# Kernel tuning notes

Hardware: AMD Instinct MI355X
Metric: run time of the kernel (lower is better)

## Reference

```python
import jax, jax.numpy as jnp
import numpy as np
import math

B, S, H = 2, 2048, 2048
NH, HD = 16, 128           # num_heads, head_dim; num_kv_heads == num_heads (MHA)
THETA = 10000.0


def setup_inputs() -> dict:
    key = jax.random.key(0)
    ks = jax.random.split(key, 5)
    scale = 0.02
    hidden_states = jax.random.normal(ks[0], (B, S, H), jnp.float32)
    q_w = jax.random.normal(ks[1], (H, H), jnp.float32) * scale
    k_w = jax.random.normal(ks[2], (H, H), jnp.float32) * scale
    v_w = jax.random.normal(ks[3], (H, H), jnp.float32) * scale
    o_w = jax.random.normal(ks[4], (H, H), jnp.float32) * scale
    # additive causal mask, finite large-negative (as HF builds it)
    causal = jnp.tril(jnp.ones((S, S), bool))
    attention_mask = jnp.where(causal, 0.0, -1e9).astype(jnp.float32)[None, None]  # [1,1,S,S]
    position_ids = jnp.broadcast_to(jnp.arange(S, dtype=jnp.int64), (B, S))
    return {
        "hidden_states": hidden_states,
        "q_w": q_w, "k_w": k_w, "v_w": v_w, "o_w": o_w,
        "attention_mask": attention_mask,
        "position_ids": position_ids,
    }


def _rotate_half(x):
    x1, x2 = x[..., : x.shape[-1] // 2], x[..., x.shape[-1] // 2 :]
    return jnp.concatenate((-x2, x1), axis=-1)


def _rope_cos_sin(position_ids):
    inv_freq = 1.0 / (THETA ** (jnp.arange(0, HD, 2, dtype=jnp.float32) / HD))  # [HD/2]
    freqs = position_ids.astype(jnp.float32)[:, :, None] * inv_freq[None, None, :]  # [B,S,HD/2]
    emb = jnp.concatenate((freqs, freqs), axis=-1)  # [B,S,HD]
    # unsqueeze head dim (unsqueeze_dim=1 after transpose to [B,H,S,D])
    return jnp.cos(emb)[:, None], jnp.sin(emb)[:, None]  # [B,1,S,HD]


def reference(hidden_states, q_w, k_w, v_w, o_w, attention_mask, position_ids):
    # projections (torch Linear: y = x @ W^T), split heads -> [B,NH,S,HD]
    def proj(w):
        return jnp.einsum('bsh,oh->bso', hidden_states, w).reshape(B, S, NH, HD).transpose(0, 2, 1, 3)
    q, k, v = proj(q_w), proj(k_w), proj(v_w)

    cos, sin = _rope_cos_sin(position_ids)
    q = q * cos + _rotate_half(q) * sin
    k = k * cos + _rotate_half(k) * sin

    scores = jnp.einsum('bhqd,bhkd->bhqk', q, k) / math.sqrt(HD)  # [B,NH,S,S]
    scores = scores + attention_mask
    attn = jax.nn.softmax(scores, axis=-1)  # dropout p=0.0 -> identity
    out = jnp.einsum('bhqk,bhkd->bhqd', attn, v)  # [B,NH,S,HD]
    out = out.transpose(0, 2, 1, 3).reshape(B, S, H)
    return jnp.einsum('bsh,oh->bso', out, o_w)
```

## Files before the change

kernel.cpp:

```cpp
#include <hip/hip_runtime.h>
#include <hip/hip_bf16.h>

using bf16 = __hip_bfloat16;
typedef short  short8  __attribute__((ext_vector_type(8)));
typedef float  float4_ __attribute__((ext_vector_type(4)));
typedef int    int4_   __attribute__((ext_vector_type(4)));

typedef __attribute__((address_space(1))) const void* gas_ptr;
typedef __attribute__((address_space(3))) void*       las_ptr;

#define MFMA_BF16(a, b, c) __builtin_amdgcn_mfma_f32_16x16x32_bf16((a), (b), (c), 0, 0, 0)

__device__ __forceinline__ float bf2f(bf16 v) { return __bfloat162float(v); }
__device__ __forceinline__ bf16  f2bf(float v) { return __float2bfloat16(v); }

#define BAR() do { asm volatile("" ::: "memory"); __builtin_amdgcn_s_barrier(); asm volatile("" ::: "memory"); } while (0)
#define WAITLGKM0() asm volatile("s_waitcnt lgkmcnt(0)" ::: "memory")

template<int CTRL>
__device__ __forceinline__ float dppmv(float x) {
    return __int_as_float(__builtin_amdgcn_update_dpp(
        0, __float_as_int(x), CTRL, 0xF, 0xF, true));
}
__device__ __forceinline__ float row16_max(float x) {
    x = fmaxf(x, dppmv<0xB1>(x));
    x = fmaxf(x, dppmv<0x4E>(x));
    x = fmaxf(x, dppmv<0x124>(x));
    x = fmaxf(x, dppmv<0x128>(x));
    return x;
}
__device__ __forceinline__ float row16_sum(float x) {
    x += dppmv<0xB1>(x);
    x += dppmv<0x4E>(x);
    x += dppmv<0x124>(x);
    x += dppmv<0x128>(x);
    return x;
}

__global__ __launch_bounds__(256)
void cvt_all(const float* __restrict__ X,  const float* __restrict__ Wq,
             const float* __restrict__ Wk, const float* __restrict__ Wv,
             const float* __restrict__ Wo,
             bf16* __restrict__ Xb,  bf16* __restrict__ Wqb,
             bf16* __restrict__ Wkb, bf16* __restrict__ Wvb,
             bf16* __restrict__ Wob)
{
    const size_t i = ((size_t)blockIdx.x * 256 + threadIdx.x) * 8;
    const float* src; bf16* dst; size_t off;
    if (i < 8388608)       { src = X;  dst = Xb;  off = i; }
    else if (i < 12582912) { src = Wq; dst = Wqb; off = i - 8388608; }
    else if (i < 16777216) { src = Wk; dst = Wkb; off = i - 12582912; }
    else if (i < 20971520) { src = Wv; dst = Wvb; off = i - 16777216; }
    else                   { src = Wo; dst = Wob; off = i - 20971520; }
    const float4_ a = *(const float4_*)(src + off);
    const float4_ b = *(const float4_*)(src + off + 4);
    union { short8 s; bf16 h[8]; } u;
#pragma unroll
    for (int j = 0; j < 4; ++j) { u.h[j] = f2bf(a[j]); u.h[j + 4] = f2bf(b[j]); }
    *(short8*)(dst + off) = u.s;
}

__global__ __launch_bounds__(512, 2)
void gemm_bn128(const bf16* __restrict__ Ap, const bf16* __restrict__ Wp,
                bf16* __restrict__ Oq, float* __restrict__ OF, int mode)
{
    constexpr int NT = 32;
    __shared__ bf16 As0[2 * 256 * 64];
    __shared__ bf16 Bs0[2 * 128 * 64];

    const int nwg  = gridDim.x * gridDim.y;
    const int bid0 = blockIdx.y * gridDim.x + blockIdx.x;
    const int cpx  = nwg >> 3;
    const int swzb = (bid0 & 7) * cpx + (bid0 >> 3);
    const int bn = (swzb % gridDim.x) * 128;
    const int bm = (swzb / gridDim.x) * 256;

    const int tid  = threadIdx.x;
    const int w    = tid >> 6;
    const int ln   = tid & 63;
    const int r15  = ln & 15;
    const int quad = ln >> 4;
    const int wr   = w >> 1;
    const int wc   = w & 1;

    const int srow = ln >> 3;
    const int scol = ((ln & 7) ^ srow) * 8;
    const int w8   = w * 8;
    const int cx   = (r15 & 7) * 8;

#define STAGE_A(pb, ts) do {                                                \
    _Pragma("unroll")                                                       \
    for (int c = 0; c < 4; ++c) {                                           \
        const int rl = c * 64 + w8;                                         \
        __builtin_amdgcn_global_load_lds(                                   \
            (gas_ptr)(Ap + (size_t)(bm + rl + srow) * 2048 + (ts) * 64 + scol), \
            (las_ptr)(As0 + (pb) * 16384 + rl * 64), 16, 0, 0);             \
    } } while (0)

#define STAGE_B0(pb, ts) do {                                               \
    const int rl = w8;                                                      \
    __builtin_amdgcn_global_load_lds(                                       \
        (gas_ptr)(Wp + (size_t)(bn + rl + srow) * 2048 + (ts) * 64 + scol), \
        (las_ptr)(Bs0 + (pb) * 8192 + rl * 64), 16, 0, 0);                  \
    } while (0)

#define STAGE_B1(pb, ts) do {                                               \
    const int rl = 64 + w8;                                                 \
    __builtin_amdgcn_global_load_lds(                                       \
        (gas_ptr)(Wp + (size_t)(bn + rl + srow) * 2048 + (ts) * 64 + scol), \
        (las_ptr)(Bs0 + (pb) * 8192 + rl * 64), 16, 0, 0);                  \
    } while (0)

#define LDA() do {                                                          \
    _Pragma("unroll")                                                       \
    for (int mi = 0; mi < 4; ++mi) {                                        \
        const int row = wr * 64 + mi * 16 + r15;                            \
        a[mi][0] = *(const short8*)(As0 + p * 16384 + row * 64 + ((quad * 8) ^ cx));      \
        a[mi][1] = *(const short8*)(As0 + p * 16384 + row * 64 + ((32 + quad * 8) ^ cx)); \
    } } while (0)

#define LDB(qn) do {                                                        \
    _Pragma("unroll")                                                       \
    for (int j = 0; j < 2; ++j) {                                           \
        const int row = wc * 64 + ((qn) * 2 + j) * 16 + r15;                \
        b[j][0] = *(const short8*)(Bs0 + p * 8192 + row * 64 + ((quad * 8) ^ cx));      \
        b[j][1] = *(const short8*)(Bs0 + p * 8192 + row * 64 + ((32 + quad * 8) ^ cx)); \
    } } while (0)

#define MM(qn) do {                                                         \
    __builtin_amdgcn_s_setprio(1);                                          \
    _Pragma("unroll")                                                       \
    for (int mi = 0; mi < 4; ++mi)                                          \
        _Pragma("unroll")                                                   \
        for (int j = 0; j < 2; ++j)                                         \
            _Pragma("unroll")                                               \
            for (int kk = 0; kk < 2; ++kk)                                  \
                acc[mi][(qn) * 2 + j] =                                     \
                    MFMA_BF16(a[mi][kk], b[j][kk], acc[mi][(qn) * 2 + j]);  \
    __builtin_amdgcn_s_setprio(0); } while (0)

    float4_ acc[4][4];
    const float4_ fzero = {0.f, 0.f, 0.f, 0.f};
#pragma unroll
    for (int i = 0; i < 4; ++i)
#pragma unroll
        for (int j = 0; j < 4; ++j) acc[i][j] = fzero;

    short8 a[4][2], b[2][2];

    STAGE_A(0, 0); STAGE_B0(0, 0); STAGE_B1(0, 0);
    STAGE_A(1, 1); STAGE_B0(1, 1);
    asm volatile("s_waitcnt vmcnt(5)" ::: "memory");
    BAR();

    for (int t = 0; t < NT; ++t) {
        const int p = t & 1, pq = p ^ 1;
        LDA(); LDB(0);
        if (t + 1 < NT) STAGE_B1(pq, t + 1);
        asm volatile("s_waitcnt lgkmcnt(8)" ::: "memory");
        BAR(); WAITLGKM0();
        MM(0);
        BAR();
        LDB(1);
        if (t + 2 < NT) { STAGE_A(p, t + 2); STAGE_B0(p, t + 2); }
        BAR(); WAITLGKM0();
        MM(1);
        if (t >= NT - 2) { asm volatile("s_waitcnt vmcnt(0)" ::: "memory"); }
        else             { asm volatile("s_waitcnt vmcnt(5)" ::: "memory"); }
        BAR();
    }

#pragma unroll
    for (int mi = 0; mi < 4; ++mi) {
#pragma unroll
        for (int ni = 0; ni < 4; ++ni) {
#pragma unroll
            for (int r = 0; r < 4; ++r) {
                const int row = bm + wr * 64 + mi * 16 + quad * 4 + r;
                const int col = bn + wc * 64 + ni * 16 + r15;
                const float v = acc[mi][ni][r];
                if (mode == 0) {
                    const int z = col >> 11, c2 = col & 2047;
                    const int h = c2 >> 7, d = c2 & 127;
                    const int bb = row >> 11, s = row & 2047;
                    Oq[(size_t)z * 8388608 + (((size_t)bb * 16 + h) * 2048 + s) * 128 + d] = f2bf(v);
                } else {
                    OF[(size_t)row * 2048 + col] = v;
                }
            }
        }
    }
#undef STAGE_A
#undef STAGE_B0
#undef STAGE_B1
#undef LDA
#undef LDB
#undef MM
}

__global__ __launch_bounds__(256)
void rope_scale(bf16* __restrict__ Q, bf16* __restrict__ Kb)
{
    const int idx = blockIdx.x * 256 + threadIdx.x;
    const int d  = idx & 63;
    const int s  = (idx >> 6) & 2047;
    const int bh = idx >> 17;
    const size_t base = ((size_t)bh * 2048 + s) * 128;

    const float inv_freq = expf(-(float)d * (9.210340371976184f / 64.f));
    const float ang = (float)s * inv_freq;
    const float c = cosf(ang), sn = sinf(ang);
    const float sc = 0.08838834764831845f;

    const float q1 = bf2f(Q[base + d]), q2 = bf2f(Q[base + d + 64]);
    Q[base + d]      = f2bf((q1 * c - q2 * sn) * sc);
    Q[base + d + 64] = f2bf((q2 * c + q1 * sn) * sc);

    const float k1 = bf2f(Kb[base + d]), k2 = bf2f(Kb[base + d + 64]);
    Kb[base + d]      = f2bf(k1 * c - k2 * sn);
    Kb[base + d + 64] = f2bf(k2 * c + k1 * sn);
}

__global__ __launch_bounds__(512)
void flash_attn(const bf16* __restrict__ Qg, const bf16* __restrict__ Kg,
                const bf16* __restrict__ Vg, bf16* __restrict__ Og)
{
    constexpr int S = 2048;
    const int pr = blockIdx.x;
    const int bh = blockIdx.y;
    const int b = bh >> 4, h = bh & 15;
    const size_t base = (size_t)bh * S * 128;
    const bf16* Qp = Qg + base;
    const bf16* Kp = Kg + base;
    const bf16* Vp = Vg + base;

    const int tid  = threadIdx.x;
    const int wave = tid >> 6;
    const int ln   = tid & 63;
    const int r15  = ln & 15;
    const int quad = ln >> 4;
    const int sid  = wave & 3;
    const int hi   = wave >> 2;

    __shared__ bf16 Ks[64][136];
    __shared__ bf16 Vt[128][72];
    __shared__ bf16 Ps[8][32][72];

    const int strip = hi ? (15 - pr) : pr;
    const int qrow0 = strip * 128 + sid * 32;
    const int dt    = qrow0 >> 6;
    const int ktmax = 2 * (15 - pr) + 1;

    short8 qf[2][4];
#pragma unroll
    for (int rf = 0; rf < 2; ++rf)
#pragma unroll
        for (int ks = 0; ks < 4; ++ks)
            qf[rf][ks] = *(const short8*)&Qp[(size_t)(qrow0 + rf * 16 + r15) * 128
                                             + ks * 32 + quad * 8];

    float4_ acc_o[2][8];
    const float4_ fzero = {0.f, 0.f, 0.f, 0.f};
#pragma unroll
    for (int rf = 0; rf < 2; ++rf)
#pragma unroll
        for (int of = 0; of < 8; ++of) acc_o[rf][of] = fzero;
    float m_run[2][4], l_run[2][4];
#pragma unroll
    for (int rf = 0; rf < 2; ++rf)
#pragma unroll
        for (int r = 0; r < 4; ++r) { m_run[rf][r] = -__builtin_inff(); l_run[rf][r] = 0.f; }

    const int kr = tid >> 4;
    const int kc = (tid & 15) * 8;
    const int vd = wave * 16;

    {
#pragma unroll
        for (int p = 0; p < 2; ++p)
            *(int4_*)&Ks[kr + p * 32][kc] =
                *(const int4_*)&Kp[(size_t)(kr + p * 32) * 128 + kc];
        union { int4_ v; bf16 h[8]; } u;
#pragma unroll
        for (int p = 0; p < 2; ++p) {
            u.v = *(const int4_*)&Vp[(size_t)ln * 128 + vd + p * 8];
#pragma unroll
            for (int j = 0; j < 8; ++j)
                Vt[vd + p * 8 + j][ln] = u.h[j];
        }
    }
    __syncthreads();

    for (int kt = 0; kt <= ktmax; ++kt) {
        const bool more = (kt < ktmax);

        int4_ kpre0, kpre1, vpre0, vpre1;
        if (more) {
            const int krow = (kt + 1) * 64;
            kpre0 = *(const int4_*)&Kp[(size_t)(krow + kr) * 128 + kc];
            kpre1 = *(const int4_*)&Kp[(size_t)(krow + kr + 32) * 128 + kc];
            vpre0 = *(const int4_*)&Vp[(size_t)(krow + ln) * 128 + vd];
            vpre1 = *(const int4_*)&Vp[(size_t)(krow + ln) * 128 + vd + 8];
        }

        if (kt <= dt) {
            float4_ sacc[2][4];
            __builtin_amdgcn_s_setprio(1);
#pragma unroll
            for (int nf = 0; nf < 4; ++nf) {
                sacc[0][nf] = fzero;
                sacc[1][nf] = fzero;
#pragma unroll
                for (int ks = 0; ks < 4; ++ks) {
                    short8 kf = *(const short8*)&Ks[nf * 16 + r15][ks * 32 + quad * 8];
                    sacc[0][nf] = MFMA_BF16(qf[0][ks], kf, sacc[0][nf]);
                    sacc[1][nf] = MFMA_BF16(qf[1][ks], kf, sacc[1][nf]);
                }
            }
            __builtin_amdgcn_s_setprio(0);

            if (kt == dt) {
#pragma unroll
                for (int rf = 0; rf < 2; ++rf) {
                    const int ro = (qrow0 & 63) + rf * 16 + quad * 4;
#pragma unroll
                    for (int nf = 0; nf < 4; ++nf) {
                        const int col = nf * 16 + r15;
#pragma unroll
                        for (int r = 0; r < 4; ++r)
                            if (col > ro + r) sacc[rf][nf][r] = -__builtin_inff();
                    }
                }
            }

#pragma unroll
            for (int rf = 0; rf < 2; ++rf) {
                float rm4[4];
                float g = 0.f;
#pragma unroll
                for (int r = 0; r < 4; ++r) {
                    float rm = fmaxf(fmaxf(sacc[rf][0][r], sacc[rf][1][r]),
                                     fmaxf(sacc[rf][2][r], sacc[rf][3][r]));
                    rm4[r] = row16_max(rm);
                    g = fmaxf(g, rm4[r] - m_run[rf][r]);
                }
                const bool resc = !__all(g <= 8.f);
                float mnew[4], alpha[4];
                if (resc) {
#pragma unroll
                    for (int r = 0; r < 4; ++r) {
                        mnew[r]  = fmaxf(m_run[rf][r], rm4[r]);
                        alpha[r] = __expf(m_run[rf][r] - mnew[r]);
                        m_run[rf][r] = mnew[r];
                    }
                } else {
#pragma unroll
                    for (int r = 0; r < 4; ++r) { mnew[r] = m_run[rf][r]; alpha[r] = 1.f; }
                }
                float rs[4] = {0.f, 0.f, 0.f, 0.f};
#pragma unroll
                for (int nf = 0; nf < 4; ++nf) {
#pragma unroll
                    for (int r = 0; r < 4; ++r) {
                        const float pp = __expf(sacc[rf][nf][r] - mnew[r]);
                        rs[r] += pp;
                        Ps[wave][rf * 16 + quad * 4 + r][nf * 16 + r15] = f2bf(pp);
                    }
                }
#pragma unroll
                for (int r = 0; r < 4; ++r) {
                    const float t = row16_sum(rs[r]);
                    l_run[rf][r] = resc ? (l_run[rf][r] * alpha[r] + t)
                                        : (l_run[rf][r] + t);
                }
                if (resc) {
#pragma unroll
                    for (int of = 0; of < 8; ++of)
#pragma unroll
                        for (int r = 0; r < 4; ++r)
                            acc_o[rf][of][r] *= alpha[r];
                }
            }

            __builtin_amdgcn_s_setprio(1);
#pragma unroll
            for (int k2 = 0; k2 < 2; ++k2) {
                short8 pf0 = *(const short8*)&Ps[wave][r15][k2 * 32 + quad * 8];
                short8 pf1 = *(const short8*)&Ps[wave][16 + r15][k2 * 32 + quad * 8];
#pragma unroll
                for (int of = 0; of < 8; ++of) {
                    short8 vf = *(const short8*)&Vt[of * 16 + r15][k2 * 32 + quad * 8];
                    acc_o[0][of] = MFMA_BF16(pf0, vf, acc_o[0][of]);
                    acc_o[1][of] = MFMA_BF16(pf1, vf, acc_o[1][of]);
                }
            }
            __builtin_amdgcn_s_setprio(0);
        }

        __syncthreads();
        if (more) {
            *(int4_*)&Ks[kr][kc]      = kpre0;
            *(int4_*)&Ks[kr + 32][kc] = kpre1;
            union { int4_ v; bf16 h[8]; } u;
            u.v = vpre0;
#pragma unroll
            for (int j = 0; j < 8; ++j) Vt[vd + j][ln] = u.h[j];
            u.v = vpre1;
#pragma unroll
            for (int j = 0; j < 8; ++j) Vt[vd + 8 + j][ln] = u.h[j];
        }
        __syncthreads();
    }

#pragma unroll
    for (int rf = 0; rf < 2; ++rf) {
#pragma unroll
        for (int r = 0; r < 4; ++r) {
            const float inv = 1.f / l_run[rf][r];
            const int  s  = qrow0 + rf * 16 + quad * 4 + r;
            const size_t ob = (((size_t)b * S + s) * 16 + h) * 128;
#pragma unroll
            for (int of = 0; of < 8; ++of)
                Og[ob + of * 16 + r15] = f2bf(acc_o[rf][of][r] * inv);
        }
    }
}

extern "C" void kernel_launch(void* const* d_in, const int* in_sizes, int n_in,
                              void* d_out, int out_size, void* d_ws, size_t ws_size,
                              hipStream_t stream)
{
    const float* X  = (const float*)d_in[0];
    const float* Wq = (const float*)d_in[1];
    const float* Wk = (const float*)d_in[2];
    const float* Wv = (const float*)d_in[3];
    const float* Wo = (const float*)d_in[4];
    float* out = (float*)d_out;

    bf16* Xb  = (bf16*)d_ws;
    bf16* Wqb = Xb  + 8388608;
    bf16* Wkb = Wqb + 4194304;
    bf16* Wvb = Wkb + 4194304;
    bf16* Wob = Wvb + 4194304;
    bf16* q   = Wob + 4194304;
    bf16* k   = q   + 8388608;
    bf16* v   = k   + 8388608;
    bf16* ao  = v   + 8388608;

    dim3 blk(256);
    cvt_all<<<dim3(12288), blk, 0, stream>>>(X, Wq, Wk, Wv, Wo,
                                             Xb, Wqb, Wkb, Wvb, Wob);
    gemm_bn128<<<dim3(48, 16), dim3(512), 0, stream>>>(Xb, Wqb, q, nullptr, 0);
    rope_scale<<<dim3((2 * 16 * 2048 * 64) / 256), blk, 0, stream>>>(q, k);
    flash_attn<<<dim3(8, 32), dim3(512), 0, stream>>>(q, k, v, ao);
    gemm_bn128<<<dim3(16, 16), dim3(512), 0, stream>>>(ao, Wob, nullptr, out, 1);
}
```

Measured before the change: 421.7 us.

## Restructure flash attention into 256-thread blocks pairing 64-row strips; tabulate RoPE

Flash attention now launches 16x32 blocks of 4 waves. Each wave handles a 16-row slice of a low query strip and a 16-row slice of its mirrored high strip, and the high strip alone keeps running after the low strip hits its diagonal, which keeps causal work balanced at a finer 64-row granularity. K/V staging is spread across fewer threads, each doing more loads. A separate kernel precomputes a RoPE cos/sin table so rope_scale does not call expf/sinf/cosf per element, at the cost of an extra launch and table reads. The smaller blocks and extra grid may change occupancy and double the K/V reload traffic per head.

```diff
diff --git a/kernel.cpp b/kernel.cpp
--- a/kernel.cpp
+++ b/kernel.cpp
@@ -199,7 +199,19 @@
 }
 
 __global__ __launch_bounds__(256)
-void rope_scale(bf16* __restrict__ Q, bf16* __restrict__ Kb)
+void rope_tab(float2* __restrict__ tab)
+{
+    const int i = blockIdx.x * 256 + threadIdx.x;
+    const int d = i & 63;
+    const int s = i >> 6;
+    const float inv_freq = expf(-(float)d * (9.210340371976184f / 64.f));
+    const float ang = (float)s * inv_freq;
+    tab[i] = make_float2(cosf(ang), sinf(ang));
+}
+
+__global__ __launch_bounds__(256)
+void rope_scale(bf16* __restrict__ Q, bf16* __restrict__ Kb,
+                const float2* __restrict__ tab)
 {
     const int idx = blockIdx.x * 256 + threadIdx.x;
     const int d  = idx & 63;
@@ -207,9 +219,8 @@
     const int bh = idx >> 17;
     const size_t base = ((size_t)bh * 2048 + s) * 128;
 
-    const float inv_freq = expf(-(float)d * (9.210340371976184f / 64.f));
-    const float ang = (float)s * inv_freq;
-    const float c = cosf(ang), sn = sinf(ang);
+    const float2 cs = tab[s * 64 + d];
+    const float c = cs.x, sn = cs.y;
     const float sc = 0.08838834764831845f;
 
     const float q1 = bf2f(Q[base + d]), q2 = bf2f(Q[base + d + 64]);
@@ -221,12 +232,12 @@
     Kb[base + d + 64] = f2bf(k2 * c + k1 * sn);
 }
 
-__global__ __launch_bounds__(512)
+__global__ __launch_bounds__(256)
 void flash_attn(const bf16* __restrict__ Qg, const bf16* __restrict__ Kg,
                 const bf16* __restrict__ Vg, bf16* __restrict__ Og)
 {
     constexpr int S = 2048;
-    const int pr = blockIdx.x;
+    const int p  = blockIdx.x;
     const int bh = blockIdx.y;
     const int b = bh >> 4, h = bh & 15;
     const size_t base = (size_t)bh * S * 128;
@@ -239,25 +250,23 @@
     const int ln   = tid & 63;
     const int r15  = ln & 15;
     const int quad = ln >> 4;
-    const int sid  = wave & 3;
-    const int hi   = wave >> 2;
 
     __shared__ bf16 Ks[64][136];
     __shared__ bf16 Vt[128][72];
-    __shared__ bf16 Ps[8][32][72];
-
-    const int strip = hi ? (15 - pr) : pr;
-    const int qrow0 = strip * 128 + sid * 32;
-    const int dt    = qrow0 >> 6;
-    const int ktmax = 2 * (15 - pr) + 1;
+    __shared__ bf16 Ps[4][32][72];
+
+    const int qlo   = p * 64 + wave * 16;
+    const int qhi   = (31 - p) * 64 + wave * 16;
+    const int dtlo  = p;
+    const int ktmax = 31 - p;
+    const int ro    = wave * 16 + quad * 4;
 
     short8 qf[2][4];
 #pragma unroll
-    for (int rf = 0; rf < 2; ++rf)
-#pragma unroll
-        for (int ks = 0; ks < 4; ++ks)
-            qf[rf][ks] = *(const short8*)&Qp[(size_t)(qrow0 + rf * 16 + r15) * 128
-                                             + ks * 32 + quad * 8];
+    for (int ks = 0; ks < 4; ++ks) {
+        qf[0][ks] = *(const short8*)&Qp[(size_t)(qlo + r15) * 128 + ks * 32 + quad * 8];
+        qf[1][ks] = *(const short8*)&Qp[(size_t)(qhi + r15) * 128 + ks * 32 + quad * 8];
+    }
 
     float4_ acc_o[2][8];
     const float4_ fzero = {0.f, 0.f, 0.f, 0.f};
@@ -273,43 +282,96 @@
 
     const int kr = tid >> 4;
     const int kc = (tid & 15) * 8;
-    const int vd = wave * 16;
+    const int vd = wave * 32;
 
     {
 #pragma unroll
-        for (int p = 0; p < 2; ++p)
-            *(int4_*)&Ks[kr + p * 32][kc] =
-                *(const int4_*)&Kp[(size_t)(kr + p * 32) * 128 + kc];
+        for (int pp = 0; pp < 4; ++pp)
+            *(int4_*)&Ks[kr + pp * 16][kc] =
+                *(const int4_*)&Kp[(size_t)(kr + pp * 16) * 128 + kc];
         union { int4_ v; bf16 h[8]; } u;
 #pragma unroll
-        for (int p = 0; p < 2; ++p) {
-            u.v = *(const int4_*)&Vp[(size_t)ln * 128 + vd + p * 8];
+        for (int pp = 0; pp < 4; ++pp) {
+            u.v = *(const int4_*)&Vp[(size_t)ln * 128 + vd + pp * 8];
 #pragma unroll
             for (int j = 0; j < 8; ++j)
-                Vt[vd + p * 8 + j][ln] = u.h[j];
+                Vt[vd + pp * 8 + j][ln] = u.h[j];
         }
     }
     __syncthreads();
+
+#define SOFTMAX(rfi) do {                                                   \
+        float rm4[4]; float g = 0.f;                                        \
+        _Pragma("unroll")                                                   \
+        for (int r = 0; r < 4; ++r) {                                       \
+            float rm = fmaxf(fmaxf(sacc[rfi][0][r], sacc[rfi][1][r]),       \
+                             fmaxf(sacc[rfi][2][r], sacc[rfi][3][r]));      \
+            rm4[r] = row16_max(rm);                                         \
+            g = fmaxf(g, rm4[r] - m_run[rfi][r]);                           \
+        }                                                                   \
+        const bool resc = !__all(g <= 8.f);                                 \
+        float mnew[4];                                                      \
+        if (resc) {                                                         \
+            float alpha[4];                                                 \
+            _Pragma("unroll")                                               \
+            for (int r = 0; r < 4; ++r) {                                   \
+                mnew[r]  = fmaxf(m_run[rfi][r], rm4[r]);                    \
+                alpha[r] = __expf(m_run[rfi][r] - mnew[r]);                 \
+                m_run[rfi][r] = mnew[r];                                    \
+            }                                                               \
+            _Pragma("unroll")                                               \
+            for (int r = 0; r < 4; ++r) l_run[rfi][r] *= alpha[r];          \
+            _Pragma("unroll")                                               \
+            for (int of = 0; of < 8; ++of)                                  \
+                _Pragma("unroll")                                           \
+                for (int r = 0; r < 4; ++r)                                 \
+                    acc_o[rfi][of][r] *= alpha[r];                          \
+        } else {                                                            \
+            _Pragma("unroll")                                               \
+            for (int r = 0; r < 4; ++r) mnew[r] = m_run[rfi][r];            \
+        }                                                                   \
+        float rs[4] = {0.f, 0.f, 0.f, 0.f};                                 \
+        _Pragma("unroll")                                                   \
+        for (int nf = 0; nf < 4; ++nf)                                      \
+            _Pragma("unroll")                                               \
+            for (int r = 0; r < 4; ++r) {                                   \
+                const float pp2 = __expf(sacc[rfi][nf][r] - mnew[r]);       \
+                rs[r] += pp2;                                               \
+                Ps[wave][(rfi) * 16 + quad * 4 + r][nf * 16 + r15] = f2bf(pp2); \
+            }                                                               \
+        _Pragma("unroll")                                                   \
+        for (int r = 0; r < 4; ++r) l_run[rfi][r] += row16_sum(rs[r]);      \
+    } while (0)
+
+#define DIAGMASK(rfi) do {                                                  \
+        _Pragma("unroll")                                                   \
+        for (int nf = 0; nf < 4; ++nf) {                                    \
+            const int col = nf * 16 + r15;                                  \
+            _Pragma("unroll")                                               \
+            for (int r = 0; r < 4; ++r)                                     \
+                if (col > ro + r) sacc[rfi][nf][r] = -__builtin_inff();     \
+        }                                                                   \
+    } while (0)
 
     for (int kt = 0; kt <= ktmax; ++kt) {
         const bool more = (kt < ktmax);
 
-        int4_ kpre0, kpre1, vpre0, vpre1;
+        int4_ kpre[4], vpre[4];
         if (more) {
             const int krow = (kt + 1) * 64;
-            kpre0 = *(const int4_*)&Kp[(size_t)(krow + kr) * 128 + kc];
-            kpre1 = *(const int4_*)&Kp[(size_t)(krow + kr + 32) * 128 + kc];
-            vpre0 = *(const int4_*)&Vp[(size_t)(krow + ln) * 128 + vd];
-            vpre1 = *(const int4_*)&Vp[(size_t)(krow + ln) * 128 + vd + 8];
-        }
-
-        if (kt <= dt) {
-            float4_ sacc[2][4];
+#pragma unroll
+            for (int pp = 0; pp < 4; ++pp) {
+                kpre[pp] = *(const int4_*)&Kp[(size_t)(krow + kr + pp * 16) * 128 + kc];
+                vpre[pp] = *(const int4_*)&Vp[(size_t)(krow + ln) * 128 + vd + pp * 8];
+            }
+        }
+
+        float4_ sacc[2][4];
+        if (kt <= dtlo) {
             __builtin_amdgcn_s_setprio(1);
 #pragma unroll
             for (int nf = 0; nf < 4; ++nf) {
-                sacc[0][nf] = fzero;
-                sacc[1][nf] = fzero;
+                sacc[0][nf] = fzero; sacc[1][nf] = fzero;
 #pragma unroll
                 for (int ks = 0; ks < 4; ++ks) {
                     short8 kf = *(const short8*)&Ks[nf * 16 + r15][ks * 32 + quad * 8];
@@ -318,70 +380,9 @@
                 }
             }
             __builtin_amdgcn_s_setprio(0);
-
-            if (kt == dt) {
-#pragma unroll
-                for (int rf = 0; rf < 2; ++rf) {
-                    const int ro = (qrow0 & 63) + rf * 16 + quad * 4;
-#pragma unroll
-                    for (int nf = 0; nf < 4; ++nf) {
-                        const int col = nf * 16 + r15;
-#pragma unroll
-                        for (int r = 0; r < 4; ++r)
-                            if (col > ro + r) sacc[rf][nf][r] = -__builtin_inff();
-                    }
-                }
-            }
-
-#pragma unroll
-            for (int rf = 0; rf < 2; ++rf) {
-                float rm4[4];
-                float g = 0.f;
-#pragma unroll
-                for (int r = 0; r < 4; ++r) {
-                    float rm = fmaxf(fmaxf(sacc[rf][0][r], sacc[rf][1][r]),
-                                     fmaxf(sacc[rf][2][r], sacc[rf][3][r]));
-                    rm4[r] = row16_max(rm);
-                    g = fmaxf(g, rm4[r] - m_run[rf][r]);
-                }
-                const bool resc = !__all(g <= 8.f);
-                float mnew[4], alpha[4];
-                if (resc) {
-#pragma unroll
-                    for (int r = 0; r < 4; ++r) {
-                        mnew[r]  = fmaxf(m_run[rf][r], rm4[r]);
-                        alpha[r] = __expf(m_run[rf][r] - mnew[r]);
-                        m_run[rf][r] = mnew[r];
-                    }
-                } else {
-#pragma unroll
-                    for (int r = 0; r < 4; ++r) { mnew[r] = m_run[rf][r]; alpha[r] = 1.f; }
-                }
-                float rs[4] = {0.f, 0.f, 0.f, 0.f};
-#pragma unroll
-                for (int nf = 0; nf < 4; ++nf) {
-#pragma unroll
-                    for (int r = 0; r < 4; ++r) {
-                        const float pp = __expf(sacc[rf][nf][r] - mnew[r]);
-                        rs[r] += pp;
-                        Ps[wave][rf * 16 + quad * 4 + r][nf * 16 + r15] = f2bf(pp);
-                    }
-                }
-#pragma unroll
-                for (int r = 0; r < 4; ++r) {
-                    const float t = row16_sum(rs[r]);
-                    l_run[rf][r] = resc ? (l_run[rf][r] * alpha[r] + t)
-                                        : (l_run[rf][r] + t);
-                }
-                if (resc) {
-#pragma unroll
-                    for (int of = 0; of < 8; ++of)
-#pragma unroll
-                        for (int r = 0; r < 4; ++r)
-                            acc_o[rf][of][r] *= alpha[r];
-                }
-            }
-
+            if (kt == dtlo) DIAGMASK(0);
+            SOFTMAX(0);
+            SOFTMAX(1);
             __builtin_amdgcn_s_setprio(1);
 #pragma unroll
             for (int k2 = 0; k2 < 2; ++k2) {
@@ -395,29 +396,58 @@
                 }
             }
             __builtin_amdgcn_s_setprio(0);
+        } else {
+            __builtin_amdgcn_s_setprio(1);
+#pragma unroll
+            for (int nf = 0; nf < 4; ++nf) {
+                sacc[1][nf] = fzero;
+#pragma unroll
+                for (int ks = 0; ks < 4; ++ks) {
+                    short8 kf = *(const short8*)&Ks[nf * 16 + r15][ks * 32 + quad * 8];
+                    sacc[1][nf] = MFMA_BF16(qf[1][ks], kf, sacc[1][nf]);
+                }
+            }
+            __builtin_amdgcn_s_setprio(0);
+            if (kt == ktmax) DIAGMASK(1);
+            SOFTMAX(1);
+            __builtin_amdgcn_s_setprio(1);
+#pragma unroll
+            for (int k2 = 0; k2 < 2; ++k2) {
+                short8 pf1 = *(const short8*)&Ps[wave][16 + r15][k2 * 32 + quad * 8];
+#pragma unroll
+                for (int of = 0; of < 8; ++of) {
+                    short8 vf = *(const short8*)&Vt[of * 16 + r15][k2 * 32 + quad * 8];
+                    acc_o[1][of] = MFMA_BF16(pf1, vf, acc_o[1][of]);
+                }
+            }
+            __builtin_amdgcn_s_setprio(0);
         }
 
         __syncthreads();
         if (more) {
-            *(int4_*)&Ks[kr][kc]      = kpre0;
-            *(int4_*)&Ks[kr + 32][kc] = kpre1;
+#pragma unroll
+            for (int pp = 0; pp < 4; ++pp)
+                *(int4_*)&Ks[kr + pp * 16][kc] = kpre[pp];
             union { int4_ v; bf16 h[8]; } u;
-            u.v = vpre0;
-#pragma unroll
-            for (int j = 0; j < 8; ++j) Vt[vd + j][ln] = u.h[j];
-            u.v = vpre1;
-#pragma unroll
-            for (int j = 0; j < 8; ++j) Vt[vd + 8 + j][ln] = u.h[j];
+#pragma unroll
+            for (int pp = 0; pp < 4; ++pp) {
+                u.v = vpre[pp];
+#pragma unroll
+                for (int j = 0; j < 8; ++j) Vt[vd + pp * 8 + j][ln] = u.h[j];
+            }
         }
         __syncthreads();
     }
+#undef SOFTMAX
+#undef DIAGMASK
 
 #pragma unroll
     for (int rf = 0; rf < 2; ++rf) {
+        const int q0 = rf ? qhi : qlo;
 #pragma unroll
         for (int r = 0; r < 4; ++r) {
             const float inv = 1.f / l_run[rf][r];
-            const int  s  = qrow0 + rf * 16 + quad * 4 + r;
+            const int  s  = q0 + quad * 4 + r;
             const size_t ob = (((size_t)b * S + s) * 16 + h) * 128;
 #pragma unroll
             for (int of = 0; of < 8; ++of)
@@ -446,12 +476,14 @@
     bf16* k   = q   + 8388608;
     bf16* v   = k   + 8388608;
     bf16* ao  = v   + 8388608;
+    float2* tab = (float2*)(ao + 8388608);
 
     dim3 blk(256);
+    rope_tab<<<dim3(512), blk, 0, stream>>>(tab);
     cvt_all<<<dim3(12288), blk, 0, stream>>>(X, Wq, Wk, Wv, Wo,
                                              Xb, Wqb, Wkb, Wvb, Wob);
     gemm_bn128<<<dim3(48, 16), dim3(512), 0, stream>>>(Xb, Wqb, q, nullptr, 0);
-    rope_scale<<<dim3((2 * 16 * 2048 * 64) / 256), blk, 0, stream>>>(q, k);
-    flash_attn<<<dim3(8, 32), dim3(512), 0, stream>>>(q, k, v, ao);
+    rope_scale<<<dim3((2 * 16 * 2048 * 64) / 256), blk, 0, stream>>>(q, k, tab);
+    flash_attn<<<dim3(16, 32), blk, 0, stream>>>(q, k, v, ao);
     gemm_bn128<<<dim3(16, 16), dim3(512), 0, stream>>>(ao, Wob, nullptr, out, 1);
 }
```

Result: slower. 487.6 us (+15.6%).

## Split GEMM k-step into four quadrant MFMA phases and precompute RoPE table

Applied to the files above, without the earlier changes.

The GEMM main loop now loads A and B fragments in halves and issues four 2x2 MFMA quadrants, interleaving the next-stage global-to-LDS loads (B0, B1, A) between them. The aim is smaller LDS read bursts and more even overlap of memory and compute, at the cost of extra barriers per k-step. Separately, a small kernel precomputes the cos/sin table once per call, so rope_scale reads it instead of evaluating expf/cosf/sinf for every element. This adds one extra launch and a table read.

```diff
diff --git a/kernel.cpp b/kernel.cpp
--- a/kernel.cpp
+++ b/kernel.cpp
@@ -111,32 +111,32 @@
         (las_ptr)(Bs0 + (pb) * 8192 + rl * 64), 16, 0, 0);                  \
     } while (0)
 
-#define LDA() do {                                                          \
-    _Pragma("unroll")                                                       \
-    for (int mi = 0; mi < 4; ++mi) {                                        \
-        const int row = wr * 64 + mi * 16 + r15;                            \
-        a[mi][0] = *(const short8*)(As0 + p * 16384 + row * 64 + ((quad * 8) ^ cx));      \
-        a[mi][1] = *(const short8*)(As0 + p * 16384 + row * 64 + ((32 + quad * 8) ^ cx)); \
-    } } while (0)
-
-#define LDB(qn) do {                                                        \
+#define LDA_H(dst, hm) do {                                                 \
     _Pragma("unroll")                                                       \
     for (int j = 0; j < 2; ++j) {                                           \
-        const int row = wc * 64 + ((qn) * 2 + j) * 16 + r15;                \
-        b[j][0] = *(const short8*)(Bs0 + p * 8192 + row * 64 + ((quad * 8) ^ cx));      \
-        b[j][1] = *(const short8*)(Bs0 + p * 8192 + row * 64 + ((32 + quad * 8) ^ cx)); \
+        const int row = wr * 64 + ((hm) * 2 + j) * 16 + r15;                \
+        dst[j][0] = *(const short8*)(As0 + p * 16384 + row * 64 + ((quad * 8) ^ cx));      \
+        dst[j][1] = *(const short8*)(As0 + p * 16384 + row * 64 + ((32 + quad * 8) ^ cx)); \
     } } while (0)
 
-#define MM(qn) do {                                                         \
+#define LDB_H(dst, hn) do {                                                 \
+    _Pragma("unroll")                                                       \
+    for (int j = 0; j < 2; ++j) {                                           \
+        const int row = wc * 64 + ((hn) * 2 + j) * 16 + r15;                \
+        dst[j][0] = *(const short8*)(Bs0 + p * 8192 + row * 64 + ((quad * 8) ^ cx));      \
+        dst[j][1] = *(const short8*)(Bs0 + p * 8192 + row * 64 + ((32 + quad * 8) ^ cx)); \
+    } } while (0)
+
+#define MMQ(am, bnv, mo, no) do {                                           \
     __builtin_amdgcn_s_setprio(1);                                          \
     _Pragma("unroll")                                                       \
-    for (int mi = 0; mi < 4; ++mi)                                          \
+    for (int i = 0; i < 2; ++i)                                             \
         _Pragma("unroll")                                                   \
         for (int j = 0; j < 2; ++j)                                         \
             _Pragma("unroll")                                               \
             for (int kk = 0; kk < 2; ++kk)                                  \
-                acc[mi][(qn) * 2 + j] =                                     \
-                    MFMA_BF16(a[mi][kk], b[j][kk], acc[mi][(qn) * 2 + j]);  \
+                acc[(mo) * 2 + i][(no) * 2 + j] =                           \
+                    MFMA_BF16(am[i][kk], bnv[j][kk], acc[(mo) * 2 + i][(no) * 2 + j]); \
     __builtin_amdgcn_s_setprio(0); } while (0)
 
     float4_ acc[4][4];
@@ -146,27 +146,34 @@
 #pragma unroll
         for (int j = 0; j < 4; ++j) acc[i][j] = fzero;
 
-    short8 a[4][2], b[2][2];
+    short8 a0[2][2], a1[2][2], b0[2][2], b1[2][2];
 
     STAGE_A(0, 0); STAGE_B0(0, 0); STAGE_B1(0, 0);
-    STAGE_A(1, 1); STAGE_B0(1, 1);
-    asm volatile("s_waitcnt vmcnt(5)" ::: "memory");
+    STAGE_A(1, 1); STAGE_B0(1, 1); STAGE_B1(1, 1);
+    asm volatile("s_waitcnt vmcnt(6)" ::: "memory");
     BAR();
 
     for (int t = 0; t < NT; ++t) {
-        const int p = t & 1, pq = p ^ 1;
-        LDA(); LDB(0);
-        if (t + 1 < NT) STAGE_B1(pq, t + 1);
-        asm volatile("s_waitcnt lgkmcnt(8)" ::: "memory");
+        const int p = t & 1;
+        LDA_H(a0, 0); LDB_H(b0, 0);
         BAR(); WAITLGKM0();
-        MM(0);
+        MMQ(a0, b0, 0, 0);
         BAR();
-        LDB(1);
-        if (t + 2 < NT) { STAGE_A(p, t + 2); STAGE_B0(p, t + 2); }
+        LDB_H(b1, 1);
+        if (t + 2 < NT) STAGE_B0(p, t + 2);
         BAR(); WAITLGKM0();
-        MM(1);
+        MMQ(a0, b1, 0, 1);
+        BAR();
+        LDA_H(a1, 1);
+        if (t + 2 < NT) STAGE_B1(p, t + 2);
+        BAR(); WAITLGKM0();
+        MMQ(a1, b1, 1, 1);
+        BAR();
+        if (t + 2 < NT) STAGE_A(p, t + 2);
+        BAR();
+        MMQ(a1, b0, 1, 0);
         if (t >= NT - 2) { asm volatile("s_waitcnt vmcnt(0)" ::: "memory"); }
-        else             { asm volatile("s_waitcnt vmcnt(5)" ::: "memory"); }
+        else             { asm volatile("s_waitcnt vmcnt(6)" ::: "memory"); }
         BAR();
     }
 
@@ -193,13 +200,25 @@
 #undef STAGE_A
 #undef STAGE_B0
 #undef STAGE_B1
-#undef LDA
-#undef LDB
-#undef MM
+#undef LDA_H
+#undef LDB_H
+#undef MMQ
 }
 
 __global__ __launch_bounds__(256)
-void rope_scale(bf16* __restrict__ Q, bf16* __restrict__ Kb)
+void rope_tab(float2* __restrict__ tab)
+{
+    const int i = blockIdx.x * 256 + threadIdx.x;
+    const int d = i & 63;
+    const int s = i >> 6;
+    const float inv_freq = expf(-(float)d * (9.210340371976184f / 64.f));
+    const float ang = (float)s * inv_freq;
+    tab[i] = make_float2(cosf(ang), sinf(ang));
+}
+
+__global__ __launch_bounds__(256)
+void rope_scale(bf16* __restrict__ Q, bf16* __restrict__ Kb,
+                const float2* __restrict__ tab)
 {
     const int idx = blockIdx.x * 256 + threadIdx.x;
     const int d  = idx & 63;
@@ -207,9 +226,8 @@
     const int bh = idx >> 17;
     const size_t base = ((size_t)bh * 2048 + s) * 128;
 
-    const float inv_freq = expf(-(float)d * (9.210340371976184f / 64.f));
-    const float ang = (float)s * inv_freq;
-    const float c = cosf(ang), sn = sinf(ang);
+    const float2 cs = tab[s * 64 + d];
+    const float c = cs.x, sn = cs.y;
     const float sc = 0.08838834764831845f;
 
     const float q1 = bf2f(Q[base + d]), q2 = bf2f(Q[base + d + 64]);
@@ -446,12 +464,14 @@
     bf16* k   = q   + 8388608;
     bf16* v   = k   + 8388608;
     bf16* ao  = v   + 8388608;
+    float2* tab = (float2*)(ao + 8388608);
 
     dim3 blk(256);
+    rope_tab<<<dim3(512), blk, 0, stream>>>(tab);
     cvt_all<<<dim3(12288), blk, 0, stream>>>(X, Wq, Wk, Wv, Wo,
                                              Xb, Wqb, Wkb, Wvb, Wob);
     gemm_bn128<<<dim3(48, 16), dim3(512), 0, stream>>>(Xb, Wqb, q, nullptr, 0);
-    rope_scale<<<dim3((2 * 16 * 2048 * 64) / 256), blk, 0, stream>>>(q, k);
+    rope_scale<<<dim3((2 * 16 * 2048 * 64) / 256), blk, 0, stream>>>(q, k, tab);
     flash_attn<<<dim3(8, 32), dim3(512), 0, stream>>>(q, k, v, ao);
     gemm_bn128<<<dim3(16, 16), dim3(512), 0, stream>>>(ao, Wob, nullptr, out, 1);
 }
```

Result: slower. 470.2 us (+11.5%).

## Fuse RoPE and query scaling into the QKV GEMM epilogue via a cos/sin table

Applied to the files above, without the earlier changes.

Drops the separate rope_scale kernel, which re-read and re-wrote the whole Q and K tensors. The QKV GEMM's B-tile columns are remapped so each wave holds both the d and d+64 halves of a head, and its epilogue applies the rotation (plus the query scale for Q) before storing bf16. A 2048x64 cos/sin table is built by extra blocks appended to the conversion kernel, which avoids transcendental math in the GEMM epilogue. This saves one kernel launch and a full memory round trip, at the cost of a heavier epilogue with table loads and branches.

```diff
diff --git a/kernel.cpp b/kernel.cpp
--- a/kernel.cpp
+++ b/kernel.cpp
@@ -43,8 +43,17 @@
              const float* __restrict__ Wo,
              bf16* __restrict__ Xb,  bf16* __restrict__ Wqb,
              bf16* __restrict__ Wkb, bf16* __restrict__ Wvb,
-             bf16* __restrict__ Wob)
+             bf16* __restrict__ Wob, float2* __restrict__ tab)
 {
+    if (blockIdx.x >= 12288) {
+        const int i = (blockIdx.x - 12288) * 256 + threadIdx.x;
+        const int d = i & 63;
+        const int s = i >> 6;
+        const float inv_freq = expf(-(float)d * (9.210340371976184f / 64.f));
+        const float ang = (float)s * inv_freq;
+        tab[i] = make_float2(cosf(ang), sinf(ang));
+        return;
+    }
     const size_t i = ((size_t)blockIdx.x * 256 + threadIdx.x) * 8;
     const float* src; bf16* dst; size_t off;
     if (i < 8388608)       { src = X;  dst = Xb;  off = i; }
@@ -62,7 +71,8 @@
 
 __global__ __launch_bounds__(512, 2)
 void gemm_bn128(const bf16* __restrict__ Ap, const bf16* __restrict__ Wp,
-                bf16* __restrict__ Oq, float* __restrict__ OF, int mode)
+                bf16* __restrict__ Oq, float* __restrict__ OF,
+                const float2* __restrict__ tab, int mode)
 {
     constexpr int NT = 32;
     __shared__ bf16 As0[2 * 256 * 64];
@@ -122,7 +132,7 @@
 #define LDB(qn) do {                                                        \
     _Pragma("unroll")                                                       \
     for (int j = 0; j < 2; ++j) {                                           \
-        const int row = wc * 64 + ((qn) * 2 + j) * 16 + r15;                \
+        const int row = wc * 32 + (qn) * 64 + j * 16 + r15;                 \
         b[j][0] = *(const short8*)(Bs0 + p * 8192 + row * 64 + ((quad * 8) ^ cx));      \
         b[j][1] = *(const short8*)(Bs0 + p * 8192 + row * 64 + ((32 + quad * 8) ^ cx)); \
     } } while (0)
@@ -170,22 +180,45 @@
         BAR();
     }
 
-#pragma unroll
-    for (int mi = 0; mi < 4; ++mi) {
-#pragma unroll
-        for (int ni = 0; ni < 4; ++ni) {
-#pragma unroll
-            for (int r = 0; r < 4; ++r) {
-                const int row = bm + wr * 64 + mi * 16 + quad * 4 + r;
-                const int col = bn + wc * 64 + ni * 16 + r15;
-                const float v = acc[mi][ni][r];
-                if (mode == 0) {
-                    const int z = col >> 11, c2 = col & 2047;
-                    const int h = c2 >> 7, d = c2 & 127;
+    if (mode == 0) {
+        const int z = bn >> 11;
+        const int h = (bn >> 7) & 15;
+        bf16* Ob = Oq + (size_t)z * 8388608;
+        const float sc = 0.08838834764831845f;
+#pragma unroll
+        for (int mi = 0; mi < 4; ++mi) {
+#pragma unroll
+            for (int ni = 0; ni < 2; ++ni) {
+                const int d = wc * 32 + ni * 16 + r15;
+#pragma unroll
+                for (int r = 0; r < 4; ++r) {
+                    const int row = bm + wr * 64 + mi * 16 + quad * 4 + r;
                     const int bb = row >> 11, s = row & 2047;
-                    Oq[(size_t)z * 8388608 + (((size_t)bb * 16 + h) * 2048 + s) * 128 + d] = f2bf(v);
-                } else {
-                    OF[(size_t)row * 2048 + col] = v;
+                    float vlo = acc[mi][ni][r];
+                    float vhi = acc[mi][ni + 2][r];
+                    if (z < 2) {
+                        const float2 cs = tab[s * 64 + d];
+                        const float lo = vlo * cs.x - vhi * cs.y;
+                        const float hi = vhi * cs.x + vlo * cs.y;
+                        vlo = lo; vhi = hi;
+                        if (z == 0) { vlo *= sc; vhi *= sc; }
+                    }
+                    const size_t ob = (((size_t)bb * 16 + h) * 2048 + s) * 128 + d;
+                    Ob[ob]      = f2bf(vlo);
+                    Ob[ob + 64] = f2bf(vhi);
+                }
+            }
+        }
+    } else {
+#pragma unroll
+        for (int mi = 0; mi < 4; ++mi) {
+#pragma unroll
+            for (int ni = 0; ni < 4; ++ni) {
+                const int col = bn + wc * 32 + (ni >> 1) * 64 + (ni & 1) * 16 + r15;
+#pragma unroll
+                for (int r = 0; r < 4; ++r) {
+                    const int row = bm + wr * 64 + mi * 16 + quad * 4 + r;
+                    OF[(size_t)row * 2048 + col] = acc[mi][ni][r];
                 }
             }
         }
@@ -196,29 +229,6 @@
 #undef LDA
 #undef LDB
 #undef MM
-}
-
-__global__ __launch_bounds__(256)
-void rope_scale(bf16* __restrict__ Q, bf16* __restrict__ Kb)
-{
-    const int idx = blockIdx.x * 256 + threadIdx.x;
-    const int d  = idx & 63;
-    const int s  = (idx >> 6) & 2047;
-    const int bh = idx >> 17;
-    const size_t base = ((size_t)bh * 2048 + s) * 128;
-
-    const float inv_freq = expf(-(float)d * (9.210340371976184f / 64.f));
-    const float ang = (float)s * inv_freq;
-    const float c = cosf(ang), sn = sinf(ang);
-    const float sc = 0.08838834764831845f;
-
-    const float q1 = bf2f(Q[base + d]), q2 = bf2f(Q[base + d + 64]);
-    Q[base + d]      = f2bf((q1 * c - q2 * sn) * sc);
-    Q[base + d + 64] = f2bf((q2 * c + q1 * sn) * sc);
-
-    const float k1 = bf2f(Kb[base + d]), k2 = bf2f(Kb[base + d + 64]);
-    Kb[base + d]      = f2bf(k1 * c - k2 * sn);
-    Kb[base + d + 64] = f2bf(k2 * c + k1 * sn);
 }
 
 __global__ __launch_bounds__(512)
@@ -446,12 +456,12 @@
     bf16* k   = q   + 8388608;
     bf16* v   = k   + 8388608;
     bf16* ao  = v   + 8388608;
+    float2* tab = (float2*)(ao + 8388608);
 
     dim3 blk(256);
-    cvt_all<<<dim3(12288), blk, 0, stream>>>(X, Wq, Wk, Wv, Wo,
-                                             Xb, Wqb, Wkb, Wvb, Wob);
-    gemm_bn128<<<dim3(48, 16), dim3(512), 0, stream>>>(Xb, Wqb, q, nullptr, 0);
-    rope_scale<<<dim3((2 * 16 * 2048 * 64) / 256), blk, 0, stream>>>(q, k);
+    cvt_all<<<dim3(12800), blk, 0, stream>>>(X, Wq, Wk, Wv, Wo,
+                                             Xb, Wqb, Wkb, Wvb, Wob, tab);
+    gemm_bn128<<<dim3(48, 16), dim3(512), 0, stream>>>(Xb, Wqb, q, nullptr, tab, 0);
     flash_attn<<<dim3(8, 32), dim3(512), 0, stream>>>(q, k, v, ao);
-    gemm_bn128<<<dim3(16, 16), dim3(512), 0, stream>>>(ao, Wob, nullptr, out, 1);
-}
+    gemm_bn128<<<dim3(16, 16), dim3(512), 0, stream>>>(ao, Wob, nullptr, out, tab, 1);
+}
```

Result: no change. 418.3 us (-0.8%).
